# Kernel optimization log

Measured on AMD Instinct MI355X. Metric: run time of the kernel, lower is better.

## Reference

```python
import jax, jax.numpy as jnp
import numpy as np

COMMITMENT_COST = 0.25
NUM_CODES = 4096
EMBED_DIM = 64


def setup_inputs() -> dict:
    key = jax.random.key(0)
    k1, k2 = jax.random.split(key)
    z_e = jax.random.normal(k1, (65536, EMBED_DIM), dtype=jnp.float32)
    embeddings = jax.random.normal(k2, (NUM_CODES, EMBED_DIM), dtype=jnp.float32)
    return {"z_e": z_e, "embeddings": embeddings}


def reference(z_e, embeddings):
    # Squared Euclidean distances; argmin is identical to torch.cdist argmin.
    # d2[n,k] = |z_e[n]|^2 - 2 z_e[n].e[k] + |e[k]|^2
    z_sq = jnp.sum(z_e * z_e, axis=-1, keepdims=True)            # [N,1]
    e_sq = jnp.sum(embeddings * embeddings, axis=-1)              # [K]
    d2 = z_sq - 2.0 * jnp.einsum('nd,kd->nk', z_e, embeddings) + e_sq  # [N,K]
    indices = jnp.argmin(d2, axis=-1)                             # [N] int
    z_q = embeddings[indices]                                     # [N,D] gather

    # commitment loss = mse(stop_grad(z_q), z_e)
    commitment_loss = COMMITMENT_COST * jnp.mean(
        (jax.lax.stop_gradient(z_q) - z_e) ** 2)

    # straight-through estimator
    z_q_st = z_e + jax.lax.stop_gradient(z_q - z_e)

    # code usage stats: one-hot mean == normalized histogram (scatter-add)
    n = z_e.shape[0]
    counts = jnp.zeros((NUM_CODES,), dtype=jnp.float32).at[indices].add(1.0)
    avg_probs = counts / n
    perplexity = jnp.exp(-jnp.sum(avg_probs * jnp.log(avg_probs + 1e-10)))
    n_active = jnp.sum(avg_probs > 0.001)

    return z_q_st, indices, commitment_loss, perplexity, n_active
```

## Files before the change

### kernel.cpp

```cpp
#include <hip/hip_runtime.h>
#include <math.h>

#define D 64
#define K 4096
#define MARGIN 0.08f
#define KSPLIT 4
#define CPH (K / 16 / KSPLIT)

typedef float f32x4 __attribute__((ext_vector_type(4)));
typedef _Float16 f16x8 __attribute__((ext_vector_type(8)));

__global__ __launch_bounds__(256) void esq_kernel(const float* __restrict__ emb,
                                                  float* __restrict__ e_sq) {
  int k = blockIdx.x * 256 + threadIdx.x;
  if (k >= K) return;
  const float* e = emb + (size_t)k * D;
  float s = 0.f;
#pragma unroll
  for (int d = 0; d < D; ++d) s = fmaf(e[d], e[d], s);
  e_sq[k] = s;
}

__global__ __launch_bounds__(256) void esplit_kernel(const float* __restrict__ emb,
                                                     short* __restrict__ e_h) {
  int i = blockIdx.x * 256 + threadIdx.x;
  if (i >= (K / 16) * 2 * 64) return;
  int lane = i & 63;
  int t = (i >> 6) & 1;
  int c = i >> 7;
  int quad = lane >> 4, col = lane & 15;
  const float* src = emb + (size_t)(c * 16 + col) * D + t * 32 + quad * 8;
  f32x4 u0 = *(const f32x4*)src;
  f32x4 u1 = *(const f32x4*)(src + 4);
  f16x8 h;
#pragma unroll
  for (int j = 0; j < 8; ++j) {
    float x = (j < 4) ? u0[j] : u1[j - 4];
    h[j] = (_Float16)x;
  }
  *(f16x8*)(e_h + (size_t)i * 8) = h;
}

__global__ __launch_bounds__(256, 2) void dist_kernel(const float* __restrict__ z_e,
                                                      const short* __restrict__ e_h,
                                                      const float* __restrict__ esq,
                                                      float* __restrict__ pbest,
                                                      float* __restrict__ psec,
                                                      int* __restrict__ pidx) {
  const int tid = threadIdx.x;
  const int wv = tid >> 6;
  const int lane = tid & 63;
  const int quad = lane >> 4, col = lane & 15;
  const int rowbase = blockIdx.x * 128 + wv * 32;
  const int half = blockIdx.y;
  const int c0 = half * CPH;

  f16x8 a_hi[2][2], a_lo[2][2];
#pragma unroll
  for (int s = 0; s < 2; ++s) {
#pragma unroll
    for (int t = 0; t < 2; ++t) {
      const float* zr = z_e + (size_t)(rowbase + s * 16 + col) * D + t * 32 + quad * 8;
      f32x4 u0 = *(const f32x4*)zr;
      f32x4 u1 = *(const f32x4*)(zr + 4);
#pragma unroll
      for (int j = 0; j < 8; ++j) {
        float x = (j < 4) ? u0[j] : u1[j - 4];
        _Float16 h = (_Float16)x;
        a_hi[s][t][j] = h;
        a_lo[s][t][j] = (_Float16)(x - (float)h);
      }
    }
  }

  float best[8], second[8];
  int bidx[8];
#pragma unroll
  for (int i = 0; i < 8; ++i) {
    best[i] = -__builtin_inff();
    second[i] = -__builtin_inff();
    bidx[i] = 0;
  }

  const short* pB = e_h + (size_t)c0 * 1024 + (size_t)lane * 8;
  const float* pE = esq + c0 * 16 + col;
  f16x8 b0 = *(const f16x8*)pB;
  f16x8 b1 = *(const f16x8*)(pB + 512);
  float eq = *pE;
  int code = c0 * 16 + col;

  for (int cc = 0; cc < CPH; ++cc) {
    pB += 1024;
    pE += 16;
    f16x8 n0 = *(const f16x8*)pB;
    f16x8 n1 = *(const f16x8*)(pB + 512);
    float neq = *pE;

    const float seed = -0.5f * eq;
    f32x4 acc0 = {seed, seed, seed, seed};
    f32x4 acc1 = acc0;
    acc0 = __builtin_amdgcn_mfma_f32_16x16x32_f16(a_hi[0][0], b0, acc0, 0, 0, 0);
    acc1 = __builtin_amdgcn_mfma_f32_16x16x32_f16(a_hi[1][0], b0, acc1, 0, 0, 0);
    acc0 = __builtin_amdgcn_mfma_f32_16x16x32_f16(a_lo[0][0], b0, acc0, 0, 0, 0);
    acc1 = __builtin_amdgcn_mfma_f32_16x16x32_f16(a_lo[1][0], b0, acc1, 0, 0, 0);
    acc0 = __builtin_amdgcn_mfma_f32_16x16x32_f16(a_hi[0][1], b1, acc0, 0, 0, 0);
    acc1 = __builtin_amdgcn_mfma_f32_16x16x32_f16(a_hi[1][1], b1, acc1, 0, 0, 0);
    acc0 = __builtin_amdgcn_mfma_f32_16x16x32_f16(a_lo[0][1], b1, acc0, 0, 0, 0);
    acc1 = __builtin_amdgcn_mfma_f32_16x16x32_f16(a_lo[1][1], b1, acc1, 0, 0, 0);

#pragma unroll
    for (int r = 0; r < 4; ++r) {
      float q = acc0[r];
      float ob = best[r];
      best[r] = fmaxf(ob, q);
      second[r] = __builtin_amdgcn_fmed3f(ob, q, second[r]);
      bidx[r] = (q > ob) ? code : bidx[r];
    }
#pragma unroll
    for (int r = 0; r < 4; ++r) {
      float q = acc1[r];
      float ob = best[4 + r];
      best[4 + r] = fmaxf(ob, q);
      second[4 + r] = __builtin_amdgcn_fmed3f(ob, q, second[4 + r]);
      bidx[4 + r] = (q > ob) ? code : bidx[4 + r];
    }

    b0 = n0;
    b1 = n1;
    eq = neq;
    code += 16;
  }

#pragma unroll
  for (int i = 0; i < 8; ++i) {
    float b = -2.f * best[i];
    float s2 = -2.f * second[i];
    int ix = bidx[i];
#pragma unroll
    for (int off = 1; off < 16; off <<= 1) {
      float ob = __shfl_xor(b, off);
      float os = __shfl_xor(s2, off);
      int oi = __shfl_xor(ix, off);
      float ns = fminf(fminf(s2, os), fmaxf(b, ob));
      if (ob < b || (ob == b && oi < ix)) ix = oi;
      b = fminf(b, ob);
      s2 = ns;
    }
    if (col == 0) {
      int row = rowbase + (i >> 2) * 16 + quad * 4 + (i & 3);
      size_t o = (size_t)half * 65536 + row;
      pbest[o] = b;
      psec[o] = s2;
      pidx[o] = ix;
    }
  }
}

__global__ __launch_bounds__(256) void merge_kernel(const float* __restrict__ pbest,
                                                    const float* __restrict__ psec,
                                                    const int* __restrict__ pidx,
                                                    int* __restrict__ best_idx,
                                                    int* __restrict__ worklist,
                                                    int* __restrict__ nwork,
                                                    int N) {
  int row = blockIdx.x * 256 + threadIdx.x;
  float b = pbest[row];
  float s2 = psec[row];
  int ix = pidx[row];
#pragma unroll
  for (int h = 1; h < KSPLIT; ++h) {
    size_t o = (size_t)h * 65536 + row;
    float bh = pbest[o];
    float sh = psec[o];
    int ih = pidx[o];
    s2 = fminf(fminf(s2, sh), fmaxf(b, bh));
    if (bh < b) ix = ih;
    b = fminf(b, bh);
  }
  best_idx[row] = ix;
  if (s2 - b < MARGIN) {
    int slot = atomicAdd(nwork, 1);
    worklist[slot] = row;
  }
}

__global__ __launch_bounds__(256, 1) void resolve_kernel(const float* __restrict__ z_e,
                                                         const float* __restrict__ emb,
                                                         const float* __restrict__ esq,
                                                         const float* __restrict__ pbest,
                                                         const float* __restrict__ psec,
                                                         const int* __restrict__ pidx,
                                                         const int* __restrict__ worklist,
                                                         const int* __restrict__ nwork,
                                                         int* __restrict__ best_idx) {
  const int tid = threadIdx.x;
  const int wave = tid >> 6;
  const int lane = tid & 63;
  const int wgid = blockIdx.x * 4 + wave;
  const int wstep = gridDim.x * 4;

  __shared__ float zs[4][D];
  const int n = *nwork;

  for (int j = wgid; j < n; j += wstep) {
    const int row = worklist[j];
    if (lane < 16) ((f32x4*)zs[wave])[lane] = *((const f32x4*)(z_e + (size_t)row * D) + lane);

    float pb[KSPLIT], ps[KSPLIT];
    int pi[KSPLIT];
    float B = __builtin_inff();
#pragma unroll
    for (int h = 0; h < KSPLIT; ++h) {
      size_t o = (size_t)h * 65536 + row;
      pb[h] = pbest[o];
      ps[h] = psec[o];
      pi[h] = pidx[o];
      B = fminf(B, pb[h]);
    }
    const float lim = B + MARGIN;

    float bv = __builtin_inff();
    int bi = 0;
#pragma unroll
    for (int h = 0; h < KSPLIT; ++h) {
      if (ps[h] < lim) {
        float hb = __builtin_inff();
        int hx = 0;
        for (int t = 0; t < 16; ++t) {
          int c = h * 1024 + t * 64 + lane;
          const f32x4* er = (const f32x4*)(emb + (size_t)c * D);
          f32x4 a = {0.f, 0.f, 0.f, 0.f};
#pragma unroll
          for (int i = 0; i < 16; ++i)
            a = __builtin_elementwise_fma(er[i], ((const f32x4*)zs[wave])[i], a);
          float dot = (a[0] + a[1]) + (a[2] + a[3]);
          float q = fmaf(-2.f, dot, esq[c]);
          if (q < hb) { hb = q; hx = c; }
        }
#pragma unroll
        for (int off = 32; off > 0; off >>= 1) {
          float ov = __shfl_down(hb, off);
          int oi = __shfl_down(hx, off);
          if (ov < hb || (ov == hb && oi < hx)) { hb = ov; hx = oi; }
        }
        hb = __shfl(hb, 0);
        hx = __shfl(hx, 0);
        if (hb < bv || (hb == bv && hx < bi)) { bv = hb; bi = hx; }
      } else if (pb[h] < lim) {
        int c = pi[h];
        float p = emb[(size_t)c * D + lane] * zs[wave][lane];
#pragma unroll
        for (int off = 1; off < 64; off <<= 1) p += __shfl_xor(p, off);
        float q = fmaf(-2.f, p, esq[c]);
        if (q < bv || (q == bv && c < bi)) { bv = q; bi = c; }
      }
    }
    if (lane == 0) best_idx[row] = bi;
  }
}

__global__ __launch_bounds__(256) void finalize_kernel(const float* __restrict__ z_e,
                                                       const float* __restrict__ emb,
                                                       const int* __restrict__ best_idx,
                                                       float* __restrict__ out_zq,
                                                       float* __restrict__ out_idx,
                                                       int* __restrict__ counts,
                                                       float* __restrict__ block_loss) {
  const int tid = threadIdx.x;
  const int wave = tid >> 6;
  const int lane = tid & 63;
  const int row = blockIdx.x * 4 + wave;

  int bidx = best_idx[row];
  float ze = z_e[(size_t)row * D + lane];
  float zq = emb[(size_t)bidx * D + lane];
  float st = ze + (zq - ze);
  out_zq[(size_t)row * D + lane] = st;

  float diff = zq - ze;
  float sq = diff * diff;
#pragma unroll
  for (int off = 32; off > 0; off >>= 1) sq += __shfl_down(sq, off);

  __shared__ float ls[4];
  if (lane == 0) {
    ls[wave] = sq;
    out_idx[row] = (float)bidx;
    atomicAdd(&counts[bidx], 1);
  }
  __syncthreads();
  if (tid == 0) block_loss[blockIdx.x] = ls[0] + ls[1] + ls[2] + ls[3];
}

__global__ __launch_bounds__(1024) void stats_kernel(const float* __restrict__ block_loss,
                                                     int nblocks,
                                                     const int* __restrict__ counts,
                                                     float* __restrict__ out_scalars,
                                                     int N) {
  const int tid = threadIdx.x;
  const int wave = tid >> 6;
  const int lane = tid & 63;

  float lsum = 0.f;
  for (int i = tid; i < nblocks; i += 1024) lsum += block_loss[i];

  float ent = 0.f;
  int act = 0;
  const float invN = 1.0f / (float)N;
  for (int k = tid; k < K; k += 1024) {
    float p = (float)counts[k] * invN;
    ent += p * logf(p + 1e-10f);
    act += (p > 0.001f) ? 1 : 0;
  }

#pragma unroll
  for (int off = 32; off > 0; off >>= 1) {
    lsum += __shfl_down(lsum, off);
    ent += __shfl_down(ent, off);
    act += __shfl_down(act, off);
  }

  __shared__ float sl[16], se[16];
  __shared__ int sa[16];
  if (lane == 0) { sl[wave] = lsum; se[wave] = ent; sa[wave] = act; }
  __syncthreads();
  if (tid == 0) {
    float L = 0.f, E = 0.f;
    int A = 0;
#pragma unroll
    for (int w = 0; w < 16; ++w) { L += sl[w]; E += se[w]; A += sa[w]; }
    out_scalars[0] = 0.25f * L / ((float)N * (float)D);
    out_scalars[1] = expf(-E);
    out_scalars[2] = (float)A;
  }
}

extern "C" void kernel_launch(void* const* d_in, const int* in_sizes, int n_in,
                              void* d_out, int out_size, void* d_ws, size_t ws_size,
                              hipStream_t stream) {
  const float* z_e = (const float*)d_in[0];
  const float* emb = (const float*)d_in[1];
  const int N = in_sizes[0] / D;

  float* out = (float*)d_out;
  float* out_zq = out;
  float* out_idx = out + (size_t)N * D;
  float* out_scalars = out + (size_t)N * (D + 1);

  char* ws = (char*)d_ws;
  size_t o = 0;
  int* counts = (int*)(ws + o);      o += 16384;
  int* nwork = (int*)(ws + o);       o += 256;
  float* esq = (float*)(ws + o);     o += 16384;
  short* e_h = (short*)(ws + o);     o += (size_t)K * D * 2;
  o += 4096;
  float* pbest = (float*)(ws + o);   o += (size_t)KSPLIT * N * 4;
  float* psec = (float*)(ws + o);    o += (size_t)KSPLIT * N * 4;
  int* pidx = (int*)(ws + o);        o += (size_t)KSPLIT * N * 4;
  int* best_idx = (int*)(ws + o);    o += (size_t)N * 4;
  int* worklist = (int*)(ws + o);    o += (size_t)N * 4;
  float* block_loss = (float*)(ws + o);

  hipMemsetAsync(counts, 0, 16384 + 256, stream);

  esq_kernel<<<K / 256, 256, 0, stream>>>(emb, esq);
  esplit_kernel<<<(K / 16) * 2 * 64 / 256, 256, 0, stream>>>(emb, e_h);
  dist_kernel<<<dim3(N / 128, KSPLIT), 256, 0, stream>>>(z_e, e_h, esq,
                                                         pbest, psec, pidx);
  merge_kernel<<<N / 256, 256, 0, stream>>>(pbest, psec, pidx, best_idx,
                                            worklist, nwork, N);
  resolve_kernel<<<512, 256, 0, stream>>>(z_e, emb, esq, pbest, psec, pidx,
                                          worklist, nwork, best_idx);
  finalize_kernel<<<N / 4, 256, 0, stream>>>(z_e, emb, best_idx, out_zq, out_idx,
                                             counts, block_loss);
  stats_kernel<<<1, 1024, 0, stream>>>(block_loss, N / 4, counts, out_scalars, N);
}
```

Baseline: 230.3 us.

## Fuse esq into esplit, merge into resolve, drop memset and global worklist

Folds the embedding squared-norm computation and the counts zeroing into the esplit kernel, which removes one launch and the memset. It fuses merge and resolve into one kernel that builds a per-block worklist in shared memory instead of a global atomic worklist. The dist kernel also stores a local chunk index instead of a running code counter, which saves a register and an add per iteration. The cost is that resolve work is now bound to the block that found the ambiguous rows, which can leave blocks unevenly loaded when near-ties cluster.

```diff
diff --git a/kernel.cpp b/kernel.cpp
--- a/kernel.cpp
+++ b/kernel.cpp
@@ -10,35 +10,35 @@
 typedef float f32x4 __attribute__((ext_vector_type(4)));
 typedef _Float16 f16x8 __attribute__((ext_vector_type(8)));
 
-__global__ __launch_bounds__(256) void esq_kernel(const float* __restrict__ emb,
-                                                  float* __restrict__ e_sq) {
-  int k = blockIdx.x * 256 + threadIdx.x;
-  if (k >= K) return;
-  const float* e = emb + (size_t)k * D;
-  float s = 0.f;
-#pragma unroll
-  for (int d = 0; d < D; ++d) s = fmaf(e[d], e[d], s);
-  e_sq[k] = s;
-}
-
 __global__ __launch_bounds__(256) void esplit_kernel(const float* __restrict__ emb,
-                                                     short* __restrict__ e_h) {
+                                                     short* __restrict__ e_h,
+                                                     float* __restrict__ e_sq,
+                                                     int* __restrict__ counts) {
   int i = blockIdx.x * 256 + threadIdx.x;
-  if (i >= (K / 16) * 2 * 64) return;
-  int lane = i & 63;
-  int t = (i >> 6) & 1;
-  int c = i >> 7;
-  int quad = lane >> 4, col = lane & 15;
-  const float* src = emb + (size_t)(c * 16 + col) * D + t * 32 + quad * 8;
-  f32x4 u0 = *(const f32x4*)src;
-  f32x4 u1 = *(const f32x4*)(src + 4);
-  f16x8 h;
-#pragma unroll
-  for (int j = 0; j < 8; ++j) {
-    float x = (j < 4) ? u0[j] : u1[j - 4];
-    h[j] = (_Float16)x;
-  }
-  *(f16x8*)(e_h + (size_t)i * 8) = h;
+  {
+    int lane = i & 63;
+    int t = (i >> 6) & 1;
+    int c = i >> 7;
+    int quad = lane >> 4, col = lane & 15;
+    const float* src = emb + (size_t)(c * 16 + col) * D + t * 32 + quad * 8;
+    f32x4 u0 = *(const f32x4*)src;
+    f32x4 u1 = *(const f32x4*)(src + 4);
+    f16x8 h;
+#pragma unroll
+    for (int j = 0; j < 8; ++j) {
+      float x = (j < 4) ? u0[j] : u1[j - 4];
+      h[j] = (_Float16)x;
+    }
+    *(f16x8*)(e_h + (size_t)i * 8) = h;
+  }
+  if (i < K) {
+    counts[i] = 0;
+    const float* e = emb + (size_t)i * D;
+    float s = 0.f;
+#pragma unroll
+    for (int d = 0; d < D; ++d) s = fmaf(e[d], e[d], s);
+    e_sq[i] = s;
+  }
 }
 
 __global__ __launch_bounds__(256, 2) void dist_kernel(const float* __restrict__ z_e,
@@ -82,12 +82,12 @@
     bidx[i] = 0;
   }
 
-  const short* pB = e_h + (size_t)c0 * 1024 + (size_t)lane * 8;
+  const size_t lofs = (size_t)lane * 8;
+  const short* pB = e_h + (size_t)c0 * 1024 + lofs;
   const float* pE = esq + c0 * 16 + col;
   f16x8 b0 = *(const f16x8*)pB;
   f16x8 b1 = *(const f16x8*)(pB + 512);
   float eq = *pE;
-  int code = c0 * 16 + col;
 
   for (int cc = 0; cc < CPH; ++cc) {
     pB += 1024;
@@ -98,7 +98,7 @@
 
     const float seed = -0.5f * eq;
     f32x4 acc0 = {seed, seed, seed, seed};
-    f32x4 acc1 = acc0;
+    f32x4 acc1 = {seed, seed, seed, seed};
     acc0 = __builtin_amdgcn_mfma_f32_16x16x32_f16(a_hi[0][0], b0, acc0, 0, 0, 0);
     acc1 = __builtin_amdgcn_mfma_f32_16x16x32_f16(a_hi[1][0], b0, acc1, 0, 0, 0);
     acc0 = __builtin_amdgcn_mfma_f32_16x16x32_f16(a_lo[0][0], b0, acc0, 0, 0, 0);
@@ -110,32 +110,31 @@
 
 #pragma unroll
     for (int r = 0; r < 4; ++r) {
-      float q = acc0[r];
+      float a0 = acc0[r];
       float ob = best[r];
-      best[r] = fmaxf(ob, q);
-      second[r] = __builtin_amdgcn_fmed3f(ob, q, second[r]);
-      bidx[r] = (q > ob) ? code : bidx[r];
+      best[r] = fmaxf(ob, a0);
+      second[r] = __builtin_amdgcn_fmed3f(ob, a0, second[r]);
+      bidx[r] = (a0 > ob) ? cc : bidx[r];
     }
 #pragma unroll
     for (int r = 0; r < 4; ++r) {
-      float q = acc1[r];
+      float a1 = acc1[r];
       float ob = best[4 + r];
-      best[4 + r] = fmaxf(ob, q);
-      second[4 + r] = __builtin_amdgcn_fmed3f(ob, q, second[4 + r]);
-      bidx[4 + r] = (q > ob) ? code : bidx[4 + r];
+      best[4 + r] = fmaxf(ob, a1);
+      second[4 + r] = __builtin_amdgcn_fmed3f(ob, a1, second[4 + r]);
+      bidx[4 + r] = (a1 > ob) ? cc : bidx[4 + r];
     }
 
     b0 = n0;
     b1 = n1;
     eq = neq;
-    code += 16;
   }
 
 #pragma unroll
   for (int i = 0; i < 8; ++i) {
     float b = -2.f * best[i];
     float s2 = -2.f * second[i];
-    int ix = bidx[i];
+    int ix = (c0 + bidx[i]) * 16 + col;
 #pragma unroll
     for (int off = 1; off < 16; off <<= 1) {
       float ob = __shfl_xor(b, off);
@@ -156,54 +155,49 @@
   }
 }
 
-__global__ __launch_bounds__(256) void merge_kernel(const float* __restrict__ pbest,
-                                                    const float* __restrict__ psec,
-                                                    const int* __restrict__ pidx,
-                                                    int* __restrict__ best_idx,
-                                                    int* __restrict__ worklist,
-                                                    int* __restrict__ nwork,
-                                                    int N) {
-  int row = blockIdx.x * 256 + threadIdx.x;
-  float b = pbest[row];
-  float s2 = psec[row];
-  int ix = pidx[row];
-#pragma unroll
-  for (int h = 1; h < KSPLIT; ++h) {
-    size_t o = (size_t)h * 65536 + row;
-    float bh = pbest[o];
-    float sh = psec[o];
-    int ih = pidx[o];
-    s2 = fminf(fminf(s2, sh), fmaxf(b, bh));
-    if (bh < b) ix = ih;
-    b = fminf(b, bh);
-  }
-  best_idx[row] = ix;
-  if (s2 - b < MARGIN) {
-    int slot = atomicAdd(nwork, 1);
-    worklist[slot] = row;
-  }
-}
-
-__global__ __launch_bounds__(256, 1) void resolve_kernel(const float* __restrict__ z_e,
-                                                         const float* __restrict__ emb,
-                                                         const float* __restrict__ esq,
-                                                         const float* __restrict__ pbest,
-                                                         const float* __restrict__ psec,
-                                                         const int* __restrict__ pidx,
-                                                         const int* __restrict__ worklist,
-                                                         const int* __restrict__ nwork,
-                                                         int* __restrict__ best_idx) {
+__global__ __launch_bounds__(256) void merge_resolve_kernel(const float* __restrict__ z_e,
+                                                            const float* __restrict__ emb,
+                                                            const float* __restrict__ esq,
+                                                            const float* __restrict__ pbest,
+                                                            const float* __restrict__ psec,
+                                                            const int* __restrict__ pidx,
+                                                            int* __restrict__ best_idx) {
   const int tid = threadIdx.x;
+  __shared__ int wl[256];
+  __shared__ int wn;
+  __shared__ float zs[4][D];
+  if (tid == 0) wn = 0;
+  __syncthreads();
+
+  {
+    int row = blockIdx.x * 256 + tid;
+    float b = pbest[row];
+    float s2 = psec[row];
+    int ix = pidx[row];
+#pragma unroll
+    for (int h = 1; h < KSPLIT; ++h) {
+      size_t o = (size_t)h * 65536 + row;
+      float bh = pbest[o];
+      float sh = psec[o];
+      int ih = pidx[o];
+      s2 = fminf(fminf(s2, sh), fmaxf(b, bh));
+      if (bh < b) ix = ih;
+      b = fminf(b, bh);
+    }
+    best_idx[row] = ix;
+    if (s2 - b < MARGIN) {
+      int slot = atomicAdd(&wn, 1);
+      wl[slot] = row;
+    }
+  }
+  __syncthreads();
+
+  const int n = wn;
   const int wave = tid >> 6;
   const int lane = tid & 63;
-  const int wgid = blockIdx.x * 4 + wave;
-  const int wstep = gridDim.x * 4;
-
-  __shared__ float zs[4][D];
-  const int n = *nwork;
-
-  for (int j = wgid; j < n; j += wstep) {
-    const int row = worklist[j];
+
+  for (int j = wave; j < n; j += 4) {
+    const int row = wl[j];
     if (lane < 16) ((f32x4*)zs[wave])[lane] = *((const f32x4*)(z_e + (size_t)row * D) + lane);
 
     float pb[KSPLIT], ps[KSPLIT];
@@ -350,27 +344,21 @@
   char* ws = (char*)d_ws;
   size_t o = 0;
   int* counts = (int*)(ws + o);      o += 16384;
-  int* nwork = (int*)(ws + o);       o += 256;
+  o += 256;
   float* esq = (float*)(ws + o);     o += 16384;
   short* e_h = (short*)(ws + o);     o += (size_t)K * D * 2;
-  o += 4096;
+  o += 8192;
   float* pbest = (float*)(ws + o);   o += (size_t)KSPLIT * N * 4;
   float* psec = (float*)(ws + o);    o += (size_t)KSPLIT * N * 4;
   int* pidx = (int*)(ws + o);        o += (size_t)KSPLIT * N * 4;
   int* best_idx = (int*)(ws + o);    o += (size_t)N * 4;
-  int* worklist = (int*)(ws + o);    o += (size_t)N * 4;
   float* block_loss = (float*)(ws + o);
 
-  hipMemsetAsync(counts, 0, 16384 + 256, stream);
-
-  esq_kernel<<<K / 256, 256, 0, stream>>>(emb, esq);
-  esplit_kernel<<<(K / 16) * 2 * 64 / 256, 256, 0, stream>>>(emb, e_h);
+  esplit_kernel<<<(K / 16) * 2 * 64 / 256, 256, 0, stream>>>(emb, e_h, esq, counts);
   dist_kernel<<<dim3(N / 128, KSPLIT), 256, 0, stream>>>(z_e, e_h, esq,
                                                          pbest, psec, pidx);
-  merge_kernel<<<N / 256, 256, 0, stream>>>(pbest, psec, pidx, best_idx,
-                                            worklist, nwork, N);
-  resolve_kernel<<<512, 256, 0, stream>>>(z_e, emb, esq, pbest, psec, pidx,
-                                          worklist, nwork, best_idx);
+  merge_resolve_kernel<<<N / 256, 256, 0, stream>>>(z_e, emb, esq, pbest, psec,
+                                                    pidx, best_idx);
   finalize_kernel<<<N / 4, 256, 0, stream>>>(z_e, emb, best_idx, out_zq, out_idx,
                                              counts, block_loss);
   stats_kernel<<<1, 1024, 0, stream>>>(block_loss, N / 4, counts, out_scalars, N);
```

Result: faster. 224.9 us (-2.4%).
